# Kernel tuning notes

Measured on AMD Instinct MI355X. Metric: run time of the kernel, lower is better.

## Reference

```python
import jax, jax.numpy as jnp
import numpy as np

B, T, J, D, H = 64, 240, 22, 128, 8


def setup_inputs() -> dict:
    key = jax.random.key(0)
    ks = jax.random.split(key, 6)
    x = jax.random.normal(ks[0], (B, T, J, D), dtype=jnp.float32)
    adjacency = jax.random.randint(ks[1], (J, J), 0, 2, dtype=jnp.int32)
    # self-loops so no softmax row is fully masked (matches sane graph usage)
    adjacency = adjacency.at[jnp.arange(J), jnp.arange(J)].set(1)
    in_proj_w = jax.random.normal(ks[2], (3 * D, D), dtype=jnp.float32) * 0.05
    in_proj_b = jax.random.normal(ks[3], (3 * D,), dtype=jnp.float32) * 0.02
    out_w = jax.random.normal(ks[4], (D, D), dtype=jnp.float32) * 0.05
    out_b = jax.random.normal(ks[5], (D,), dtype=jnp.float32) * 0.02
    return {"x": x, "adjacency": adjacency, "in_proj_w": in_proj_w,
            "in_proj_b": in_proj_b, "out_w": out_w, "out_b": out_b}


def reference(x, adjacency, in_proj_w, in_proj_b, out_w, out_b):
    b, t, j, d = x.shape
    hd = d // H
    n = b * t
    x_bt = x.reshape(n, j, d)
    # combined QKV projection (nn.MultiheadAttention in_proj)
    qkv = x_bt @ in_proj_w.T + in_proj_b            # [n, j, 3d]
    q, k, v = jnp.split(qkv, 3, axis=-1)
    split_heads = lambda a: a.reshape(n, j, H, hd).transpose(0, 2, 1, 3)  # [n,H,j,hd]
    q, k, v = split_heads(q), split_heads(k), split_heads(v)
    scores = jnp.einsum('nhqd,nhkd->nhqk', q, k) / np.sqrt(hd).astype(np.float32)
    mask = adjacency <= 0                            # True = disallowed (bool attn_mask)
    scores = jnp.where(mask[None, None], -jnp.inf, scores)
    attn = jax.nn.softmax(scores, axis=-1)
    y = jnp.einsum('nhqk,nhkd->nhqd', attn, v)       # [n,H,j,hd]
    y = y.transpose(0, 2, 1, 3).reshape(n, j, d)
    y = y @ out_w.T + out_b                          # out_proj
    return y.reshape(b, t, j, d)
```

## Files before the change

kernel.cpp:

```cpp
#include <hip/hip_runtime.h>

typedef _Float16 f16;
typedef __fp16 h16x2 __attribute__((ext_vector_type(2)));
typedef _Float16 f16x4 __attribute__((ext_vector_type(4)));
typedef _Float16 f16x8 __attribute__((ext_vector_type(8)));
typedef float f32x4 __attribute__((ext_vector_type(4)));

#define N_ROWS   337920
#define RG       44
#define NGROUPS  7680
#define QKV_ROWB  512
#define QKV_BYTES (48 * QKV_ROWB)
#define VT_OFF    QKV_BYTES
#define LDS_BYTES (QKV_BYTES + 128 * 64 * 2)
#define WQKV_F16  49152
#define WOUT_F16  16384
#define MASK_OFF  ((WQKV_F16 + WOUT_F16) * 2)
#define WS_NEEDED (MASK_OFF + 4096)

__device__ __forceinline__ uint32_t swz(int row, int bytecol) {
  return (uint32_t)((row * QKV_ROWB + bytecol) ^ ((row & 7) << 4));
}
__device__ __forceinline__ uint32_t vswz(int d, int col) {
  return (uint32_t)(VT_OFF + ((d * 128 + col * 2) ^ ((d & 15) << 3)));
}
__device__ __forceinline__ f16x8 pack8z(float4 a, float4 b) {
  h16x2 p0 = __builtin_amdgcn_cvt_pkrtz(a.x, a.y);
  h16x2 p1 = __builtin_amdgcn_cvt_pkrtz(a.z, a.w);
  h16x2 p2 = __builtin_amdgcn_cvt_pkrtz(b.x, b.y);
  h16x2 p3 = __builtin_amdgcn_cvt_pkrtz(b.z, b.w);
  f16x8 r;
  r[0]=p0[0]; r[1]=p0[1]; r[2]=p1[0]; r[3]=p1[1];
  r[4]=p2[0]; r[5]=p2[1]; r[6]=p3[0]; r[7]=p3[1];
  return r;
}
__device__ __forceinline__ f16x4 pack4z(float a, float b, float c, float d) {
  h16x2 p0 = __builtin_amdgcn_cvt_pkrtz(a, b);
  h16x2 p1 = __builtin_amdgcn_cvt_pkrtz(c, d);
  f16x4 r;
  r[0]=p0[0]; r[1]=p0[1]; r[2]=p1[0]; r[3]=p1[1];
  return r;
}

__global__ void prep(const float* __restrict__ wqkv, const float* __restrict__ wout,
                     const int* __restrict__ adj, char* __restrict__ ws) {
  f16* w16 = (f16*)ws;
  int b = blockIdx.x;
  if (b < 64) {
    int i4 = (b * 256 + threadIdx.x) * 4;
    const float* src = (i4 < WQKV_F16) ? (wqkv + i4) : (wout + (i4 - WQKV_F16));
    float4 v = *(const float4*)src;
    f16x4 h;
    h[0]=(f16)v.x; h[1]=(f16)v.y; h[2]=(f16)v.z; h[3]=(f16)v.w;
    *(f16x4*)(w16 + i4) = h;
  } else {
    int t = threadIdx.x;
    int qt = t >> 7, jt = (t >> 6) & 1, l = t & 63;
    int g = l >> 4, r16 = l & 15;
    f32x4 m;
    #pragma unroll
    for (int r = 0; r < 4; r++) {
      int q = qt * 16 + r16, j = jt * 16 + 4 * g + r;
      float v = -1e30f;
      if (j < 22) v = (q >= 22 || adj[q * 22 + j] > 0) ? 0.0f : -1e30f;
      m[r] = v;
    }
    *(f32x4*)(ws + MASK_OFF + t * 16) = m;
  }
}

template <int F16M>
__global__ __launch_bounds__(256, 2)
void mga_fused(const float* __restrict__ x, const int* __restrict__ adj,
               const float* __restrict__ bqkv, const float* __restrict__ bout,
               const char* __restrict__ ws, const float* __restrict__ wqkv32,
               const float* __restrict__ wout32,
               float* __restrict__ out) {
  __shared__ __align__(16) char smem[LDS_BYTES];
  const int tid = threadIdx.x;
  const int wv = tid >> 6;
  const int l = tid & 63;
  const int g = l >> 4;
  const int r16 = l & 15;
  const long g0 = (long)blockIdx.x * RG;
  const f16* w16 = (const f16*)ws;

  {
    int d = 16 * wv + 64 * ((l >> 5) & 1) + (l & 15);
    int c0 = ((l >> 4) & 1) ? 54 : 22;
    #pragma unroll
    for (int i = 0; i < 5; i++)
      *(int*)(smem + vswz(d, c0 + 2 * i)) = 0;
  }

  f16x8 xf[3][4];
  #pragma unroll
  for (int mt = 0; mt < 3; mt++) {
    long rowg = g0 + mt * 16 + r16;
    if (rowg > (long)N_ROWS - 1) rowg = N_ROWS - 1;
    const float* xp = x + rowg * 128 + g * 8;
    #pragma unroll
    for (int ks = 0; ks < 4; ks++)
      xf[mt][ks] = pack8z(*(const float4*)(xp + ks * 32),
                          *(const float4*)(xp + ks * 32 + 4));
  }

  f16x8 wcur[4], wnxt[4];
  f32x4 bcur, bnxt;
  {
    int wrow = wv * 16 + r16;
    #pragma unroll
    for (int ks = 0; ks < 4; ks++) {
      int off = wrow * 128 + ks * 32 + g * 8;
      if (F16M) wcur[ks] = *(const f16x8*)(w16 + off);
      else      wcur[ks] = pack8z(*(const float4*)(wqkv32 + off),
                                  *(const float4*)(wqkv32 + off + 4));
    }
    bcur = *(const f32x4*)(bqkv + wv * 16 + 4 * g);
  }
  #pragma unroll
  for (int i = 0; i < 6; i++) {
    int nt = wv + 4 * i;
    if (i < 5) {
      int wrow = (nt + 4) * 16 + r16;
      #pragma unroll
      for (int ks = 0; ks < 4; ks++) {
        int off = wrow * 128 + ks * 32 + g * 8;
        if (F16M) wnxt[ks] = *(const f16x8*)(w16 + off);
        else      wnxt[ks] = pack8z(*(const float4*)(wqkv32 + off),
                                    *(const float4*)(wqkv32 + off + 4));
      }
      bnxt = *(const f32x4*)(bqkv + (nt + 4) * 16 + 4 * g);
    }
    f32x4 acc[3] = {{0,0,0,0},{0,0,0,0},{0,0,0,0}};
    #pragma unroll
    for (int ks = 0; ks < 4; ks++) {
      acc[0] = __builtin_amdgcn_mfma_f32_16x16x32_f16(wcur[ks], xf[0][ks], acc[0], 0,0,0);
      acc[1] = __builtin_amdgcn_mfma_f32_16x16x32_f16(wcur[ks], xf[1][ks], acc[1], 0,0,0);
      acc[2] = __builtin_amdgcn_mfma_f32_16x16x32_f16(wcur[ks], xf[2][ks], acc[2], 0,0,0);
    }
    float sc = (nt < 8) ? 0.25f : 1.0f;
    f32x4 bs;
    #pragma unroll
    for (int r = 0; r < 4; r++) bs[r] = bcur[r] * sc;
    #pragma unroll
    for (int mt = 0; mt < 3; mt++) {
      int rowl = mt * 16 + r16;
      if (nt < 16) {
        f16x4 h4 = pack4z(fmaf(acc[mt][0], sc, bs[0]), fmaf(acc[mt][1], sc, bs[1]),
                          fmaf(acc[mt][2], sc, bs[2]), fmaf(acc[mt][3], sc, bs[3]));
        *(f16x4*)(smem + swz(rowl, (nt * 16 + 4 * g) * 2)) = h4;
      } else if (rowl < RG) {
        int t = rowl >= 22;
        int col = t * 32 + rowl - 22 * t;
        int dv = (nt - 16) * 16 + 4 * g;
        #pragma unroll
        for (int r = 0; r < 4; r++)
          *(f16*)(smem + vswz(dv + r, col)) = (f16)(acc[mt][r] + bcur[r]);
      }
    }
    #pragma unroll
    for (int ks = 0; ks < 4; ks++) wcur[ks] = wnxt[ks];
    bcur = bnxt;
  }

  f32x4 mq[2][2];
  if (F16M) {
    #pragma unroll
    for (int qt = 0; qt < 2; qt++)
      #pragma unroll
      for (int jt = 0; jt < 2; jt++)
        mq[qt][jt] = *(const f32x4*)(ws + MASK_OFF + ((qt * 2 + jt) * 64 + l) * 16);
  } else {
    #pragma unroll
    for (int qt = 0; qt < 2; qt++)
      #pragma unroll
      for (int jt = 0; jt < 2; jt++)
        #pragma unroll
        for (int r = 0; r < 4; r++) {
          int q = qt * 16 + r16, j = jt * 16 + 4 * g + r;
          float m = -1e30f;
          if (j < 22) m = (q >= 22 || adj[q * 22 + j] > 0) ? 0.0f : -1e30f;
          mq[qt][jt][r] = m;
        }
  }

  __syncthreads();

  {
    const int t = wv >> 1;
    const int rbase = 22 * t;
    const int hbase = 4 * (wv & 1);
    const int rowk0 = rbase + r16;
    int rk1 = rbase + 16 + r16; if (rk1 > 47) rk1 = 47;
    const int rowk1 = rk1;
    #pragma unroll 2
    for (int hi = 0; hi < 4; hi++) {
      int h = hbase + hi;
      f16x4 kf0 = *(const f16x4*)(smem + swz(rowk0, (128 + h * 16 + 4 * g) * 2));
      f16x4 kf1 = *(const f16x4*)(smem + swz(rowk1, (128 + h * 16 + 4 * g) * 2));
      f16x4 vf0 = *(const f16x4*)(smem + vswz(h * 16 + r16, t * 32 + 4 * g));
      f16x4 vf1 = *(const f16x4*)(smem + vswz(h * 16 + r16, t * 32 + 16 + 4 * g));
      #pragma unroll
      for (int qt = 0; qt < 2; qt++) {
        int rowq = qt ? rowk1 : rowk0;
        f16x4 qf = *(const f16x4*)(smem + swz(rowq, (h * 16 + 4 * g) * 2));
        f32x4 z = {0.f, 0.f, 0.f, 0.f};
        f32x4 s0 = __builtin_amdgcn_mfma_f32_16x16x16f16(kf0, qf, z, 0, 0, 0);
        f32x4 s1 = __builtin_amdgcn_mfma_f32_16x16x16f16(kf1, qf, z, 0, 0, 0);
        float p[8];
        #pragma unroll
        for (int r = 0; r < 4; r++) {
          p[r]     = __expf(s0[r] + mq[qt][0][r]);
          p[4 + r] = __expf(s1[r] + mq[qt][1][r]);
        }
        float sum = ((p[0] + p[1]) + (p[2] + p[3])) + ((p[4] + p[5]) + (p[6] + p[7]));
        sum += __shfl_xor(sum, 16, 64);
        sum += __shfl_xor(sum, 32, 64);
        f16x4 pb0 = pack4z(p[0], p[1], p[2], p[3]);
        f16x4 pb1 = pack4z(p[4], p[5], p[6], p[7]);
        f32x4 ya = __builtin_amdgcn_mfma_f32_16x16x16f16(vf0, pb0, z, 0, 0, 0);
        ya = __builtin_amdgcn_mfma_f32_16x16x16f16(vf1, pb1, ya, 0, 0, 0);
        float inv = __builtin_amdgcn_rcpf(sum);
        int q = qt * 16 + r16;
        if (q < 22) {
          f16x4 yh = pack4z(ya[0] * inv, ya[1] * inv, ya[2] * inv, ya[3] * inv);
          *(f16x4*)(smem + swz(rbase + q, (h * 16 + 4 * g) * 2)) = yh;
        }
      }
    }
  }
  __syncthreads();

  const f16* w16o = w16 + WQKV_F16;
  f16x8 wf3[2][4];
  f32x4 bv3[2];
  #pragma unroll
  for (int i = 0; i < 2; i++) {
    int wrow = (2 * wv + i) * 16 + r16;
    #pragma unroll
    for (int ks = 0; ks < 4; ks++) {
      int off = wrow * 128 + ks * 32 + g * 8;
      if (F16M) wf3[i][ks] = *(const f16x8*)(w16o + off);
      else      wf3[i][ks] = pack8z(*(const float4*)(wout32 + off),
                                    *(const float4*)(wout32 + off + 4));
    }
    bv3[i] = *(const f32x4*)(bout + (2 * wv + i) * 16 + 4 * g);
  }
  #pragma unroll
  for (int mt = 0; mt < 3; mt++) {
    f16x8 af[4];
    #pragma unroll
    for (int ks = 0; ks < 4; ks++)
      af[ks] = *(const f16x8*)(smem + swz(mt * 16 + r16, (ks * 32 + g * 8) * 2));
    int rowl = mt * 16 + r16;
    #pragma unroll
    for (int i = 0; i < 2; i++) {
      f32x4 acc = {0.f, 0.f, 0.f, 0.f};
      #pragma unroll
      for (int ks = 0; ks < 4; ks++)
        acc = __builtin_amdgcn_mfma_f32_16x16x32_f16(wf3[i][ks], af[ks], acc, 0, 0, 0);
      if (rowl < RG) {
        float4 o;
        o.x = acc[0] + bv3[i][0]; o.y = acc[1] + bv3[i][1];
        o.z = acc[2] + bv3[i][2]; o.w = acc[3] + bv3[i][3];
        *(float4*)(out + (g0 + rowl) * 128 + (2 * wv + i) * 16 + 4 * g) = o;
      }
    }
  }
}

extern "C" void kernel_launch(void* const* d_in, const int* in_sizes, int n_in,
                              void* d_out, int out_size, void* d_ws, size_t ws_size,
                              hipStream_t stream) {
  const float* x    = (const float*)d_in[0];
  const int*   adj  = (const int*)d_in[1];
  const float* wqkv = (const float*)d_in[2];
  const float* bqkv = (const float*)d_in[3];
  const float* wout = (const float*)d_in[4];
  const float* bout = (const float*)d_in[5];
  float* o = (float*)d_out;

  int f16m = (d_ws != nullptr && ws_size >= (size_t)WS_NEEDED) ? 1 : 0;
  if (f16m) {
    prep<<<dim3(65), dim3(256), 0, stream>>>(wqkv, wout, adj, (char*)d_ws);
    mga_fused<1><<<dim3(NGROUPS), dim3(256), 0, stream>>>(
        x, adj, bqkv, bout, (const char*)d_ws, wqkv, wout, o);
  } else {
    mga_fused<0><<<dim3(NGROUPS), dim3(256), 0, stream>>>(
        x, adj, bqkv, bout, (const char*)d_ws, wqkv, wout, o);
  }
}
```

Baseline: 226.8 us.

## Process one 22-joint group per block instead of two

Each block now handles a single 22-row joint group: 2 M-tiles instead of 3, a smaller LDS footprint with a narrower V-transpose layout and swizzle, and the attention loop reassigned so each wave does 2 heads of the single group. Padding waste in the MFMA work drops (32 rows computed for 22 instead of 48 for 44), and the lower LDS use may allow higher occupancy. In exchange the block count doubles and the weight loads are amortised over half as many rows per block.

```diff
diff --git a/kernel.cpp b/kernel.cpp
--- a/kernel.cpp
+++ b/kernel.cpp
@@ -7,12 +7,12 @@
 typedef float f32x4 __attribute__((ext_vector_type(4)));
 
 #define N_ROWS   337920
-#define RG       44
-#define NGROUPS  7680
+#define RG       22
+#define NGROUPS  15360
 #define QKV_ROWB  512
-#define QKV_BYTES (48 * QKV_ROWB)
+#define QKV_BYTES (32 * QKV_ROWB)
 #define VT_OFF    QKV_BYTES
-#define LDS_BYTES (QKV_BYTES + 128 * 64 * 2)
+#define LDS_BYTES (QKV_BYTES + 128 * 64)
 #define WQKV_F16  49152
 #define WOUT_F16  16384
 #define MASK_OFF  ((WQKV_F16 + WOUT_F16) * 2)
@@ -22,7 +22,7 @@
   return (uint32_t)((row * QKV_ROWB + bytecol) ^ ((row & 7) << 4));
 }
 __device__ __forceinline__ uint32_t vswz(int d, int col) {
-  return (uint32_t)(VT_OFF + ((d * 128 + col * 2) ^ ((d & 15) << 3)));
+  return (uint32_t)(VT_OFF + ((d * 64 + col * 2) ^ ((d & 7) << 3)));
 }
 __device__ __forceinline__ f16x8 pack8z(float4 a, float4 b) {
   h16x2 p0 = __builtin_amdgcn_cvt_pkrtz(a.x, a.y);
@@ -87,15 +87,18 @@
 
   {
     int d = 16 * wv + 64 * ((l >> 5) & 1) + (l & 15);
-    int c0 = ((l >> 4) & 1) ? 54 : 22;
-    #pragma unroll
-    for (int i = 0; i < 5; i++)
-      *(int*)(smem + vswz(d, c0 + 2 * i)) = 0;
-  }
-
-  f16x8 xf[3][4];
-  #pragma unroll
-  for (int mt = 0; mt < 3; mt++) {
+    if (((l >> 4) & 1) == 0) {
+      #pragma unroll
+      for (int i = 0; i < 3; i++) *(int*)(smem + vswz(d, 22 + 2 * i)) = 0;
+    } else {
+      #pragma unroll
+      for (int i = 0; i < 2; i++) *(int*)(smem + vswz(d, 28 + 2 * i)) = 0;
+    }
+  }
+
+  f16x8 xf[2][4];
+  #pragma unroll
+  for (int mt = 0; mt < 2; mt++) {
     long rowg = g0 + mt * 16 + r16;
     if (rowg > (long)N_ROWS - 1) rowg = N_ROWS - 1;
     const float* xp = x + rowg * 128 + g * 8;
@@ -132,31 +135,28 @@
       }
       bnxt = *(const f32x4*)(bqkv + (nt + 4) * 16 + 4 * g);
     }
-    f32x4 acc[3] = {{0,0,0,0},{0,0,0,0},{0,0,0,0}};
+    f32x4 acc[2] = {{0,0,0,0},{0,0,0,0}};
     #pragma unroll
     for (int ks = 0; ks < 4; ks++) {
       acc[0] = __builtin_amdgcn_mfma_f32_16x16x32_f16(wcur[ks], xf[0][ks], acc[0], 0,0,0);
       acc[1] = __builtin_amdgcn_mfma_f32_16x16x32_f16(wcur[ks], xf[1][ks], acc[1], 0,0,0);
-      acc[2] = __builtin_amdgcn_mfma_f32_16x16x32_f16(wcur[ks], xf[2][ks], acc[2], 0,0,0);
     }
     float sc = (nt < 8) ? 0.25f : 1.0f;
     f32x4 bs;
     #pragma unroll
     for (int r = 0; r < 4; r++) bs[r] = bcur[r] * sc;
     #pragma unroll
-    for (int mt = 0; mt < 3; mt++) {
+    for (int mt = 0; mt < 2; mt++) {
       int rowl = mt * 16 + r16;
       if (nt < 16) {
         f16x4 h4 = pack4z(fmaf(acc[mt][0], sc, bs[0]), fmaf(acc[mt][1], sc, bs[1]),
                           fmaf(acc[mt][2], sc, bs[2]), fmaf(acc[mt][3], sc, bs[3]));
         *(f16x4*)(smem + swz(rowl, (nt * 16 + 4 * g) * 2)) = h4;
       } else if (rowl < RG) {
-        int t = rowl >= 22;
-        int col = t * 32 + rowl - 22 * t;
         int dv = (nt - 16) * 16 + 4 * g;
         #pragma unroll
         for (int r = 0; r < 4; r++)
-          *(f16*)(smem + vswz(dv + r, col)) = (f16)(acc[mt][r] + bcur[r]);
+          *(f16*)(smem + vswz(dv + r, rowl)) = (f16)(acc[mt][r] + bcur[r]);
       }
     }
     #pragma unroll
@@ -188,19 +188,15 @@
   __syncthreads();
 
   {
-    const int t = wv >> 1;
-    const int rbase = 22 * t;
-    const int hbase = 4 * (wv & 1);
-    const int rowk0 = rbase + r16;
-    int rk1 = rbase + 16 + r16; if (rk1 > 47) rk1 = 47;
-    const int rowk1 = rk1;
-    #pragma unroll 2
-    for (int hi = 0; hi < 4; hi++) {
-      int h = hbase + hi;
+    const int rowk0 = r16;
+    const int rowk1 = 16 + r16;
+    #pragma unroll
+    for (int hi = 0; hi < 2; hi++) {
+      int h = 2 * wv + hi;
       f16x4 kf0 = *(const f16x4*)(smem + swz(rowk0, (128 + h * 16 + 4 * g) * 2));
       f16x4 kf1 = *(const f16x4*)(smem + swz(rowk1, (128 + h * 16 + 4 * g) * 2));
-      f16x4 vf0 = *(const f16x4*)(smem + vswz(h * 16 + r16, t * 32 + 4 * g));
-      f16x4 vf1 = *(const f16x4*)(smem + vswz(h * 16 + r16, t * 32 + 16 + 4 * g));
+      f16x4 vf0 = *(const f16x4*)(smem + vswz(h * 16 + r16, 4 * g));
+      f16x4 vf1 = *(const f16x4*)(smem + vswz(h * 16 + r16, 16 + 4 * g));
       #pragma unroll
       for (int qt = 0; qt < 2; qt++) {
         int rowq = qt ? rowk1 : rowk0;
@@ -225,7 +221,7 @@
         int q = qt * 16 + r16;
         if (q < 22) {
           f16x4 yh = pack4z(ya[0] * inv, ya[1] * inv, ya[2] * inv, ya[3] * inv);
-          *(f16x4*)(smem + swz(rbase + q, (h * 16 + 4 * g) * 2)) = yh;
+          *(f16x4*)(smem + swz(q, (h * 16 + 4 * g) * 2)) = yh;
         }
       }
     }
@@ -248,7 +244,7 @@
     bv3[i] = *(const f32x4*)(bout + (2 * wv + i) * 16 + 4 * g);
   }
   #pragma unroll
-  for (int mt = 0; mt < 3; mt++) {
+  for (int mt = 0; mt < 2; mt++) {
     f16x8 af[4];
     #pragma unroll
     for (int ks = 0; ks < 4; ks++)
```

After: 356.1 us. 1.57x slower.

## Make fused attention kernel persistent with register-resident weights

Applied to the files above, without the earlier changes.

Replaces the one-block-per-group launch with a persistent grid of 512 blocks that loop over the row groups. The QKV and output projection weights are loaded into registers once per block instead of once per group, and the V-padding zeroing is done once. The cost is much higher register pressure (24 f16x8 weight fragments per thread plus 8 more), which risks spills or lower occupancy. There is also an extra barrier per iteration and no overlap of the next group's x loads with the current compute.

```diff
diff --git a/kernel.cpp b/kernel.cpp
--- a/kernel.cpp
+++ b/kernel.cpp
@@ -8,7 +8,8 @@
 
 #define N_ROWS   337920
 #define RG       44
-#define NGROUPS  7680
+#define NPAIRS   7680
+#define PGRID    512
 #define QKV_ROWB  512
 #define QKV_BYTES (48 * QKV_ROWB)
 #define VT_OFF    QKV_BYTES
@@ -71,99 +72,44 @@
 
 template <int F16M>
 __global__ __launch_bounds__(256, 2)
-void mga_fused(const float* __restrict__ x, const int* __restrict__ adj,
-               const float* __restrict__ bqkv, const float* __restrict__ bout,
-               const char* __restrict__ ws, const float* __restrict__ wqkv32,
-               const float* __restrict__ wout32,
-               float* __restrict__ out) {
+void mga_persist(const float* __restrict__ x, const int* __restrict__ adj,
+                 const float* __restrict__ bqkv, const float* __restrict__ bout,
+                 const char* __restrict__ ws, const float* __restrict__ wqkv32,
+                 const float* __restrict__ wout32,
+                 float* __restrict__ out) {
   __shared__ __align__(16) char smem[LDS_BYTES];
   const int tid = threadIdx.x;
   const int wv = tid >> 6;
   const int l = tid & 63;
   const int g = l >> 4;
   const int r16 = l & 15;
-  const long g0 = (long)blockIdx.x * RG;
   const f16* w16 = (const f16*)ws;
-
-  {
-    int d = 16 * wv + 64 * ((l >> 5) & 1) + (l & 15);
-    int c0 = ((l >> 4) & 1) ? 54 : 22;
-    #pragma unroll
-    for (int i = 0; i < 5; i++)
-      *(int*)(smem + vswz(d, c0 + 2 * i)) = 0;
-  }
-
-  f16x8 xf[3][4];
+  const f16* w16o = w16 + WQKV_F16;
+
+  f16x8 wp1[6][4];
   #pragma unroll
-  for (int mt = 0; mt < 3; mt++) {
-    long rowg = g0 + mt * 16 + r16;
-    if (rowg > (long)N_ROWS - 1) rowg = N_ROWS - 1;
-    const float* xp = x + rowg * 128 + g * 8;
-    #pragma unroll
-    for (int ks = 0; ks < 4; ks++)
-      xf[mt][ks] = pack8z(*(const float4*)(xp + ks * 32),
-                          *(const float4*)(xp + ks * 32 + 4));
-  }
-
-  f16x8 wcur[4], wnxt[4];
-  f32x4 bcur, bnxt;
-  {
-    int wrow = wv * 16 + r16;
+  for (int i = 0; i < 6; i++) {
+    int wrow = (wv + 4 * i) * 16 + r16;
     #pragma unroll
     for (int ks = 0; ks < 4; ks++) {
       int off = wrow * 128 + ks * 32 + g * 8;
-      if (F16M) wcur[ks] = *(const f16x8*)(w16 + off);
-      else      wcur[ks] = pack8z(*(const float4*)(wqkv32 + off),
-                                  *(const float4*)(wqkv32 + off + 4));
-    }
-    bcur = *(const f32x4*)(bqkv + wv * 16 + 4 * g);
-  }
+      if (F16M) wp1[i][ks] = *(const f16x8*)(w16 + off);
+      else      wp1[i][ks] = pack8z(*(const float4*)(wqkv32 + off),
+                                    *(const float4*)(wqkv32 + off + 4));
+    }
+  }
+  f16x8 wf3[2][4];
   #pragma unroll
-  for (int i = 0; i < 6; i++) {
-    int nt = wv + 4 * i;
-    if (i < 5) {
-      int wrow = (nt + 4) * 16 + r16;
-      #pragma unroll
-      for (int ks = 0; ks < 4; ks++) {
-        int off = wrow * 128 + ks * 32 + g * 8;
-        if (F16M) wnxt[ks] = *(const f16x8*)(w16 + off);
-        else      wnxt[ks] = pack8z(*(const float4*)(wqkv32 + off),
-                                    *(const float4*)(wqkv32 + off + 4));
-      }
-      bnxt = *(const f32x4*)(bqkv + (nt + 4) * 16 + 4 * g);
-    }
-    f32x4 acc[3] = {{0,0,0,0},{0,0,0,0},{0,0,0,0}};
+  for (int i = 0; i < 2; i++) {
+    int wrow = (2 * wv + i) * 16 + r16;
     #pragma unroll
     for (int ks = 0; ks < 4; ks++) {
-      acc[0] = __builtin_amdgcn_mfma_f32_16x16x32_f16(wcur[ks], xf[0][ks], acc[0], 0,0,0);
-      acc[1] = __builtin_amdgcn_mfma_f32_16x16x32_f16(wcur[ks], xf[1][ks], acc[1], 0,0,0);
-      acc[2] = __builtin_amdgcn_mfma_f32_16x16x32_f16(wcur[ks], xf[2][ks], acc[2], 0,0,0);
-    }
-    float sc = (nt < 8) ? 0.25f : 1.0f;
-    f32x4 bs;
-    #pragma unroll
-    for (int r = 0; r < 4; r++) bs[r] = bcur[r] * sc;
-    #pragma unroll
-    for (int mt = 0; mt < 3; mt++) {
-      int rowl = mt * 16 + r16;
-      if (nt < 16) {
-        f16x4 h4 = pack4z(fmaf(acc[mt][0], sc, bs[0]), fmaf(acc[mt][1], sc, bs[1]),
-                          fmaf(acc[mt][2], sc, bs[2]), fmaf(acc[mt][3], sc, bs[3]));
-        *(f16x4*)(smem + swz(rowl, (nt * 16 + 4 * g) * 2)) = h4;
-      } else if (rowl < RG) {
-        int t = rowl >= 22;
-        int col = t * 32 + rowl - 22 * t;
-        int dv = (nt - 16) * 16 + 4 * g;
-        #pragma unroll
-        for (int r = 0; r < 4; r++)
-          *(f16*)(smem + vswz(dv + r, col)) = (f16)(acc[mt][r] + bcur[r]);
-      }
-    }
-    #pragma unroll
-    for (int ks = 0; ks < 4; ks++) wcur[ks] = wnxt[ks];
-    bcur = bnxt;
-  }
-
+      int off = wrow * 128 + ks * 32 + g * 8;
+      if (F16M) wf3[i][ks] = *(const f16x8*)(w16o + off);
+      else      wf3[i][ks] = pack8z(*(const float4*)(wout32 + off),
+                                    *(const float4*)(wout32 + off + 4));
+    }
+  }
   f32x4 mq[2][2];
   if (F16M) {
     #pragma unroll
@@ -185,88 +131,130 @@
         }
   }
 
-  __syncthreads();
-
   {
-    const int t = wv >> 1;
-    const int rbase = 22 * t;
-    const int hbase = 4 * (wv & 1);
-    const int rowk0 = rbase + r16;
-    int rk1 = rbase + 16 + r16; if (rk1 > 47) rk1 = 47;
-    const int rowk1 = rk1;
-    #pragma unroll 2
-    for (int hi = 0; hi < 4; hi++) {
-      int h = hbase + hi;
-      f16x4 kf0 = *(const f16x4*)(smem + swz(rowk0, (128 + h * 16 + 4 * g) * 2));
-      f16x4 kf1 = *(const f16x4*)(smem + swz(rowk1, (128 + h * 16 + 4 * g) * 2));
-      f16x4 vf0 = *(const f16x4*)(smem + vswz(h * 16 + r16, t * 32 + 4 * g));
-      f16x4 vf1 = *(const f16x4*)(smem + vswz(h * 16 + r16, t * 32 + 16 + 4 * g));
-      #pragma unroll
-      for (int qt = 0; qt < 2; qt++) {
-        int rowq = qt ? rowk1 : rowk0;
-        f16x4 qf = *(const f16x4*)(smem + swz(rowq, (h * 16 + 4 * g) * 2));
-        f32x4 z = {0.f, 0.f, 0.f, 0.f};
-        f32x4 s0 = __builtin_amdgcn_mfma_f32_16x16x16f16(kf0, qf, z, 0, 0, 0);
-        f32x4 s1 = __builtin_amdgcn_mfma_f32_16x16x16f16(kf1, qf, z, 0, 0, 0);
-        float p[8];
+    int d = 16 * wv + 64 * ((l >> 5) & 1) + (l & 15);
+    int c0 = ((l >> 4) & 1) ? 54 : 22;
+    #pragma unroll
+    for (int i = 0; i < 5; i++)
+      *(int*)(smem + vswz(d, c0 + 2 * i)) = 0;
+  }
+
+  for (int pg = blockIdx.x; pg < NPAIRS; pg += PGRID) {
+    const long g0 = (long)pg * RG;
+
+    f16x8 xf[3][4];
+    #pragma unroll
+    for (int mt = 0; mt < 3; mt++) {
+      long rowg = g0 + mt * 16 + r16;
+      if (rowg > (long)N_ROWS - 1) rowg = N_ROWS - 1;
+      const float* xp = x + rowg * 128 + g * 8;
+      #pragma unroll
+      for (int ks = 0; ks < 4; ks++)
+        xf[mt][ks] = pack8z(*(const float4*)(xp + ks * 32),
+                            *(const float4*)(xp + ks * 32 + 4));
+    }
+    #pragma unroll
+    for (int i = 0; i < 6; i++) {
+      int nt = wv + 4 * i;
+      f32x4 acc[3] = {{0,0,0,0},{0,0,0,0},{0,0,0,0}};
+      #pragma unroll
+      for (int ks = 0; ks < 4; ks++) {
+        acc[0] = __builtin_amdgcn_mfma_f32_16x16x32_f16(wp1[i][ks], xf[0][ks], acc[0], 0,0,0);
+        acc[1] = __builtin_amdgcn_mfma_f32_16x16x32_f16(wp1[i][ks], xf[1][ks], acc[1], 0,0,0);
+        acc[2] = __builtin_amdgcn_mfma_f32_16x16x32_f16(wp1[i][ks], xf[2][ks], acc[2], 0,0,0);
+      }
+      f32x4 bcur = *(const f32x4*)(bqkv + nt * 16 + 4 * g);
+      float sc = (nt < 8) ? 0.25f : 1.0f;
+      f32x4 bs;
+      #pragma unroll
+      for (int r = 0; r < 4; r++) bs[r] = bcur[r] * sc;
+      #pragma unroll
+      for (int mt = 0; mt < 3; mt++) {
+        int rowl = mt * 16 + r16;
+        if (nt < 16) {
+          f16x4 h4 = pack4z(fmaf(acc[mt][0], sc, bs[0]), fmaf(acc[mt][1], sc, bs[1]),
+                            fmaf(acc[mt][2], sc, bs[2]), fmaf(acc[mt][3], sc, bs[3]));
+          *(f16x4*)(smem + swz(rowl, (nt * 16 + 4 * g) * 2)) = h4;
+        } else if (rowl < RG) {
+          int t = rowl >= 22;
+          int col = t * 32 + rowl - 22 * t;
+          int dv = (nt - 16) * 16 + 4 * g;
+          #pragma unroll
+          for (int r = 0; r < 4; r++)
+            *(f16*)(smem + vswz(dv + r, col)) = (f16)(acc[mt][r] + bcur[r]);
+        }
+      }
+    }
+    __syncthreads();
+
+    {
+      const int t = wv >> 1;
+      const int rbase = 22 * t;
+      const int hbase = 4 * (wv & 1);
+      const int rowk0 = rbase + r16;
+      int rk1 = rbase + 16 + r16; if (rk1 > 47) rk1 = 47;
+      const int rowk1 = rk1;
+      #pragma unroll 2
+      for (int hi = 0; hi < 4; hi++) {
+        int h = hbase + hi;
+        f16x4 kf0 = *(const f16x4*)(smem + swz(rowk0, (128 + h * 16 + 4 * g) * 2));
+        f16x4 kf1 = *(const f16x4*)(smem + swz(rowk1, (128 + h * 16 + 4 * g) * 2));
+        f16x4 vf0 = *(const f16x4*)(smem + vswz(h * 16 + r16, t * 32 + 4 * g));
+        f16x4 vf1 = *(const f16x4*)(smem + vswz(h * 16 + r16, t * 32 + 16 + 4 * g));
         #pragma unroll
-        for (int r = 0; r < 4; r++) {
-          p[r]     = __expf(s0[r] + mq[qt][0][r]);
-          p[4 + r] = __expf(s1[r] + mq[qt][1][r]);
-        }
-        float sum = ((p[0] + p[1]) + (p[2] + p[3])) + ((p[4] + p[5]) + (p[6] + p[7]));
-        sum += __shfl_xor(sum, 16, 64);
-        sum += __shfl_xor(sum, 32, 64);
-        f16x4 pb0 = pack4z(p[0], p[1], p[2], p[3]);
-        f16x4 pb1 = pack4z(p[4], p[5], p[6], p[7]);
-        f32x4 ya = __builtin_amdgcn_mfma_f32_16x16x16f16(vf0, pb0, z, 0, 0, 0);
-        ya = __builtin_amdgcn_mfma_f32_16x16x16f16(vf1, pb1, ya, 0, 0, 0);
-        float inv = __builtin_amdgcn_rcpf(sum);
-        int q = qt * 16 + r16;
-        if (q < 22) {
-          f16x4 yh = pack4z(ya[0] * inv, ya[1] * inv, ya[2] * inv, ya[3] * inv);
-          *(f16x4*)(smem + swz(rbase + q, (h * 16 + 4 * g) * 2)) = yh;
-        }
-      }
-    }
-  }
-  __syncthreads();
-
-  const f16* w16o = w16 + WQKV_F16;
-  f16x8 wf3[2][4];
-  f32x4 bv3[2];
-  #pragma unroll
-  for (int i = 0; i < 2; i++) {
-    int wrow = (2 * wv + i) * 16 + r16;
-    #pragma unroll
-    for (int ks = 0; ks < 4; ks++) {
-      int off = wrow * 128 + ks * 32 + g * 8;
-      if (F16M) wf3[i][ks] = *(const f16x8*)(w16o + off);
-      else      wf3[i][ks] = pack8z(*(const float4*)(wout32 + off),
-                                    *(const float4*)(wout32 + off + 4));
-    }
-    bv3[i] = *(const f32x4*)(bout + (2 * wv + i) * 16 + 4 * g);
-  }
-  #pragma unroll
-  for (int mt = 0; mt < 3; mt++) {
-    f16x8 af[4];
-    #pragma unroll
-    for (int ks = 0; ks < 4; ks++)
-      af[ks] = *(const f16x8*)(smem + swz(mt * 16 + r16, (ks * 32 + g * 8) * 2));
-    int rowl = mt * 16 + r16;
-    #pragma unroll
-    for (int i = 0; i < 2; i++) {
-      f32x4 acc = {0.f, 0.f, 0.f, 0.f};
+        for (int qt = 0; qt < 2; qt++) {
+          int rowq = qt ? rowk1 : rowk0;
+          f16x4 qf = *(const f16x4*)(smem + swz(rowq, (h * 16 + 4 * g) * 2));
+          f32x4 z = {0.f, 0.f, 0.f, 0.f};
+          f32x4 s0 = __builtin_amdgcn_mfma_f32_16x16x16f16(kf0, qf, z, 0, 0, 0);
+          f32x4 s1 = __builtin_amdgcn_mfma_f32_16x16x16f16(kf1, qf, z, 0, 0, 0);
+          float p[8];
+          #pragma unroll
+          for (int r = 0; r < 4; r++) {
+            p[r]     = __expf(s0[r] + mq[qt][0][r]);
+            p[4 + r] = __expf(s1[r] + mq[qt][1][r]);
+          }
+          float sum = ((p[0] + p[1]) + (p[2] + p[3])) + ((p[4] + p[5]) + (p[6] + p[7]));
+          sum += __shfl_xor(sum, 16, 64);
+          sum += __shfl_xor(sum, 32, 64);
+          f16x4 pb0 = pack4z(p[0], p[1], p[2], p[3]);
+          f16x4 pb1 = pack4z(p[4], p[5], p[6], p[7]);
+          f32x4 ya = __builtin_amdgcn_mfma_f32_16x16x16f16(vf0, pb0, z, 0, 0, 0);
+          ya = __builtin_amdgcn_mfma_f32_16x16x16f16(vf1, pb1, ya, 0, 0, 0);
+          float inv = __builtin_amdgcn_rcpf(sum);
+          int q = qt * 16 + r16;
+          if (q < 22) {
+            f16x4 yh = pack4z(ya[0] * inv, ya[1] * inv, ya[2] * inv, ya[3] * inv);
+            *(f16x4*)(smem + swz(rbase + q, (h * 16 + 4 * g) * 2)) = yh;
+          }
+        }
+      }
+    }
+    __syncthreads();
+
+    #pragma unroll
+    for (int mt = 0; mt < 3; mt++) {
+      f16x8 af[4];
       #pragma unroll
       for (int ks = 0; ks < 4; ks++)
-        acc = __builtin_amdgcn_mfma_f32_16x16x32_f16(wf3[i][ks], af[ks], acc, 0, 0, 0);
-      if (rowl < RG) {
-        float4 o;
-        o.x = acc[0] + bv3[i][0]; o.y = acc[1] + bv3[i][1];
-        o.z = acc[2] + bv3[i][2]; o.w = acc[3] + bv3[i][3];
-        *(float4*)(out + (g0 + rowl) * 128 + (2 * wv + i) * 16 + 4 * g) = o;
-      }
-    }
+        af[ks] = *(const f16x8*)(smem + swz(mt * 16 + r16, (ks * 32 + g * 8) * 2));
+      int rowl = mt * 16 + r16;
+      #pragma unroll
+      for (int i = 0; i < 2; i++) {
+        f32x4 acc = {0.f, 0.f, 0.f, 0.f};
+        #pragma unroll
+        for (int ks = 0; ks < 4; ks++)
+          acc = __builtin_amdgcn_mfma_f32_16x16x32_f16(wf3[i][ks], af[ks], acc, 0, 0, 0);
+        if (rowl < RG) {
+          f32x4 bv3 = *(const f32x4*)(bout + (2 * wv + i) * 16 + 4 * g);
+          float4 o;
+          o.x = acc[0] + bv3[0]; o.y = acc[1] + bv3[1];
+          o.z = acc[2] + bv3[2]; o.w = acc[3] + bv3[3];
+          *(float4*)(out + (g0 + rowl) * 128 + (2 * wv + i) * 16 + 4 * g) = o;
+        }
+      }
+    }
+    __syncthreads();
   }
 }
 
@@ -284,10 +272,10 @@
   int f16m = (d_ws != nullptr && ws_size >= (size_t)WS_NEEDED) ? 1 : 0;
   if (f16m) {
     prep<<<dim3(65), dim3(256), 0, stream>>>(wqkv, wout, adj, (char*)d_ws);
-    mga_fused<1><<<dim3(NGROUPS), dim3(256), 0, stream>>>(
+    mga_persist<1><<<dim3(PGRID), dim3(256), 0, stream>>>(
         x, adj, bqkv, bout, (const char*)d_ws, wqkv, wout, o);
   } else {
-    mga_fused<0><<<dim3(NGROUPS), dim3(256), 0, stream>>>(
+    mga_persist<0><<<dim3(PGRID), dim3(256), 0, stream>>>(
         x, adj, bqkv, bout, (const char*)d_ws, wqkv, wout, o);
   }
 }
```

After: 428.2 us. 88.8% more time.

## Fold biases into MFMA accumulators, use exp2 softmax, transpose V projection, prefetch out weights

Applied to the files above, without the earlier changes.

Biases are now loaded as the initial MFMA accumulator values instead of being added afterwards. Q is scaled by log2(e)/4 so the softmax can use exp2 in place of expf. The V projection swaps its MFMA operands so each lane writes packed f16 pairs into the transposed V tile rather than scalar halves. Half of the out-projection weights are prefetched before the first barrier and the out-projection loop is interleaved over two accumulators. The aim is fewer ALU ops and LDS stores and better hiding of weight-load latency, at the cost of higher register pressure.

```diff
diff --git a/kernel.cpp b/kernel.cpp
--- a/kernel.cpp
+++ b/kernel.cpp
@@ -17,6 +17,7 @@
 #define WOUT_F16  16384
 #define MASK_OFF  ((WQKV_F16 + WOUT_F16) * 2)
 #define WS_NEEDED (MASK_OFF + 4096)
+#define SCQ 0.3606737602222409f
 
 __device__ __forceinline__ uint32_t swz(int row, int bytecol) {
   return (uint32_t)((row * QKV_ROWB + bytecol) ^ ((row & 7) << 4));
@@ -84,6 +85,7 @@
   const int r16 = l & 15;
   const long g0 = (long)blockIdx.x * RG;
   const f16* w16 = (const f16*)ws;
+  const f16* w16o = w16 + WQKV_F16;
 
   {
     int d = 16 * wv + 64 * ((l >> 5) & 1) + (l & 15);
@@ -106,7 +108,6 @@
   }
 
   f16x8 wcur[4], wnxt[4];
-  f32x4 bcur, bnxt;
   {
     int wrow = wv * 16 + r16;
     #pragma unroll
@@ -116,7 +117,6 @@
       else      wcur[ks] = pack8z(*(const float4*)(wqkv32 + off),
                                   *(const float4*)(wqkv32 + off + 4));
     }
-    bcur = *(const f32x4*)(bqkv + wv * 16 + 4 * g);
   }
   #pragma unroll
   for (int i = 0; i < 6; i++) {
@@ -130,38 +130,52 @@
         else      wnxt[ks] = pack8z(*(const float4*)(wqkv32 + off),
                                     *(const float4*)(wqkv32 + off + 4));
       }
-      bnxt = *(const f32x4*)(bqkv + (nt + 4) * 16 + 4 * g);
-    }
-    f32x4 acc[3] = {{0,0,0,0},{0,0,0,0},{0,0,0,0}};
-    #pragma unroll
-    for (int ks = 0; ks < 4; ks++) {
-      acc[0] = __builtin_amdgcn_mfma_f32_16x16x32_f16(wcur[ks], xf[0][ks], acc[0], 0,0,0);
-      acc[1] = __builtin_amdgcn_mfma_f32_16x16x32_f16(wcur[ks], xf[1][ks], acc[1], 0,0,0);
-      acc[2] = __builtin_amdgcn_mfma_f32_16x16x32_f16(wcur[ks], xf[2][ks], acc[2], 0,0,0);
-    }
-    float sc = (nt < 8) ? 0.25f : 1.0f;
-    f32x4 bs;
-    #pragma unroll
-    for (int r = 0; r < 4; r++) bs[r] = bcur[r] * sc;
-    #pragma unroll
-    for (int mt = 0; mt < 3; mt++) {
-      int rowl = mt * 16 + r16;
-      if (nt < 16) {
-        f16x4 h4 = pack4z(fmaf(acc[mt][0], sc, bs[0]), fmaf(acc[mt][1], sc, bs[1]),
-                          fmaf(acc[mt][2], sc, bs[2]), fmaf(acc[mt][3], sc, bs[3]));
-        *(f16x4*)(smem + swz(rowl, (nt * 16 + 4 * g) * 2)) = h4;
-      } else if (rowl < RG) {
-        int t = rowl >= 22;
-        int col = t * 32 + rowl - 22 * t;
-        int dv = (nt - 16) * 16 + 4 * g;
+    }
+    if (nt < 16) {
+      f32x4 bb = *(const f32x4*)(bqkv + nt * 16 + 4 * g);
+      f32x4 acc[3] = {bb, bb, bb};
+      #pragma unroll
+      for (int ks = 0; ks < 4; ks++) {
+        acc[0] = __builtin_amdgcn_mfma_f32_16x16x32_f16(wcur[ks], xf[0][ks], acc[0], 0,0,0);
+        acc[1] = __builtin_amdgcn_mfma_f32_16x16x32_f16(wcur[ks], xf[1][ks], acc[1], 0,0,0);
+        acc[2] = __builtin_amdgcn_mfma_f32_16x16x32_f16(wcur[ks], xf[2][ks], acc[2], 0,0,0);
+      }
+      int col = nt * 16 + 4 * g;
+      #pragma unroll
+      for (int mt = 0; mt < 3; mt++) {
+        f16x4 h4;
+        if (nt < 8)
+          h4 = pack4z(acc[mt][0] * SCQ, acc[mt][1] * SCQ,
+                      acc[mt][2] * SCQ, acc[mt][3] * SCQ);
+        else
+          h4 = pack4z(acc[mt][0], acc[mt][1], acc[mt][2], acc[mt][3]);
+        *(f16x4*)(smem + swz(mt * 16 + r16, col * 2)) = h4;
+      }
+    } else {
+      float bvs = bqkv[nt * 16 + r16];
+      f32x4 bb = {bvs, bvs, bvs, bvs};
+      f32x4 acc[3] = {bb, bb, bb};
+      #pragma unroll
+      for (int ks = 0; ks < 4; ks++) {
+        acc[0] = __builtin_amdgcn_mfma_f32_16x16x32_f16(xf[0][ks], wcur[ks], acc[0], 0,0,0);
+        acc[1] = __builtin_amdgcn_mfma_f32_16x16x32_f16(xf[1][ks], wcur[ks], acc[1], 0,0,0);
+        acc[2] = __builtin_amdgcn_mfma_f32_16x16x32_f16(xf[2][ks], wcur[ks], acc[2], 0,0,0);
+      }
+      int d = (nt - 16) * 16 + r16;
+      #pragma unroll
+      for (int mt = 0; mt < 3; mt++) {
         #pragma unroll
-        for (int r = 0; r < 4; r++)
-          *(f16*)(smem + vswz(dv + r, col)) = (f16)(acc[mt][r] + bcur[r]);
+        for (int p = 0; p < 2; p++) {
+          int rowl = mt * 16 + 4 * g + 2 * p;
+          int t = rowl >= 22;
+          int col = rowl + 10 * t;
+          h16x2 v2 = __builtin_amdgcn_cvt_pkrtz(acc[mt][2*p], acc[mt][2*p+1]);
+          *(h16x2*)(smem + vswz(d, col)) = v2;
+        }
       }
     }
     #pragma unroll
     for (int ks = 0; ks < 4; ks++) wcur[ks] = wnxt[ks];
-    bcur = bnxt;
   }
 
   f32x4 mq[2][2];
@@ -183,6 +197,15 @@
           if (j < 22) m = (q >= 22 || adj[q * 22 + j] > 0) ? 0.0f : -1e30f;
           mq[qt][jt][r] = m;
         }
+  }
+
+  f16x8 wf3a[4];
+  #pragma unroll
+  for (int ks = 0; ks < 4; ks++) {
+    int off = (2 * wv * 16 + r16) * 128 + ks * 32 + g * 8;
+    if (F16M) wf3a[ks] = *(const f16x8*)(w16o + off);
+    else      wf3a[ks] = pack8z(*(const float4*)(wout32 + off),
+                                *(const float4*)(wout32 + off + 4));
   }
 
   __syncthreads();
@@ -211,8 +234,8 @@
         float p[8];
         #pragma unroll
         for (int r = 0; r < 4; r++) {
-          p[r]     = __expf(s0[r] + mq[qt][0][r]);
-          p[4 + r] = __expf(s1[r] + mq[qt][1][r]);
+          p[r]     = __builtin_exp2f(s0[r] + mq[qt][0][r]);
+          p[4 + r] = __builtin_exp2f(s1[r] + mq[qt][1][r]);
         }
         float sum = ((p[0] + p[1]) + (p[2] + p[3])) + ((p[4] + p[5]) + (p[6] + p[7]));
         sum += __shfl_xor(sum, 16, 64);
@@ -232,21 +255,16 @@
   }
   __syncthreads();
 
-  const f16* w16o = w16 + WQKV_F16;
-  f16x8 wf3[2][4];
-  f32x4 bv3[2];
-  #pragma unroll
-  for (int i = 0; i < 2; i++) {
-    int wrow = (2 * wv + i) * 16 + r16;
-    #pragma unroll
-    for (int ks = 0; ks < 4; ks++) {
-      int off = wrow * 128 + ks * 32 + g * 8;
-      if (F16M) wf3[i][ks] = *(const f16x8*)(w16o + off);
-      else      wf3[i][ks] = pack8z(*(const float4*)(wout32 + off),
-                                    *(const float4*)(wout32 + off + 4));
-    }
-    bv3[i] = *(const f32x4*)(bout + (2 * wv + i) * 16 + 4 * g);
-  }
+  f16x8 wf3b[4];
+  #pragma unroll
+  for (int ks = 0; ks < 4; ks++) {
+    int off = ((2 * wv + 1) * 16 + r16) * 128 + ks * 32 + g * 8;
+    if (F16M) wf3b[ks] = *(const f16x8*)(w16o + off);
+    else      wf3b[ks] = pack8z(*(const float4*)(wout32 + off),
+                                *(const float4*)(wout32 + off + 4));
+  }
+  f32x4 bva = *(const f32x4*)(bout + 2 * wv * 16 + 4 * g);
+  f32x4 bvb = *(const f32x4*)(bout + (2 * wv + 1) * 16 + 4 * g);
   #pragma unroll
   for (int mt = 0; mt < 3; mt++) {
     f16x8 af[4];
@@ -254,18 +272,18 @@
     for (int ks = 0; ks < 4; ks++)
       af[ks] = *(const f16x8*)(smem + swz(mt * 16 + r16, (ks * 32 + g * 8) * 2));
     int rowl = mt * 16 + r16;
-    #pragma unroll
-    for (int i = 0; i < 2; i++) {
-      f32x4 acc = {0.f, 0.f, 0.f, 0.f};
-      #pragma unroll
-      for (int ks = 0; ks < 4; ks++)
-        acc = __builtin_amdgcn_mfma_f32_16x16x32_f16(wf3[i][ks], af[ks], acc, 0, 0, 0);
-      if (rowl < RG) {
-        float4 o;
-        o.x = acc[0] + bv3[i][0]; o.y = acc[1] + bv3[i][1];
-        o.z = acc[2] + bv3[i][2]; o.w = acc[3] + bv3[i][3];
-        *(float4*)(out + (g0 + rowl) * 128 + (2 * wv + i) * 16 + 4 * g) = o;
-      }
+    f32x4 acc0 = bva, acc1 = bvb;
+    #pragma unroll
+    for (int ks = 0; ks < 4; ks++) {
+      acc0 = __builtin_amdgcn_mfma_f32_16x16x32_f16(wf3a[ks], af[ks], acc0, 0, 0, 0);
+      acc1 = __builtin_amdgcn_mfma_f32_16x16x32_f16(wf3b[ks], af[ks], acc1, 0, 0, 0);
+    }
+    if (rowl < RG) {
+      float4 oa, ob;
+      oa.x = acc0[0]; oa.y = acc0[1]; oa.z = acc0[2]; oa.w = acc0[3];
+      ob.x = acc1[0]; ob.y = acc1[1]; ob.z = acc1[2]; ob.w = acc1[3];
+      *(float4*)(out + (g0 + rowl) * 128 + 2 * wv * 16 + 4 * g) = oa;
+      *(float4*)(out + (g0 + rowl) * 128 + (2 * wv + 1) * 16 + 4 * g) = ob;
     }
   }
 }
```

After: 226.6 us. About the same (-0.1%).
